# Kernel optimization log

Measured on AMD Instinct MI355X. Metric: run time of the kernel, lower is better.

## Reference

```python
import jax, jax.numpy as jnp
import numpy as np

HEADS = 8
DIM_HEAD = 32


def setup_inputs() -> dict:
    key = jax.random.key(0)
    k1, k2, k3, k4 = jax.random.split(key, 4)
    dim, hidden = 256, HEADS * DIM_HEAD
    x = jax.random.normal(k1, (4, dim, 48, 48), dtype=jnp.float32)
    # 1x1 conv weights stored as [out_ch, in_ch]
    w_qkv = jax.random.normal(k2, (3 * hidden, dim), dtype=jnp.float32) * (dim ** -0.5)
    w_out = jax.random.normal(k3, (dim, hidden), dtype=jnp.float32) * (hidden ** -0.5)
    b_out = jax.random.normal(k4, (dim,), dtype=jnp.float32) * 0.01
    return {"x": x, "w_qkv": w_qkv, "w_out": w_out, "b_out": b_out}


def reference(x, w_qkv, w_out, b_out):
    B, C, H, W = x.shape
    n = H * W
    scale = DIM_HEAD ** -0.5
    # 1x1 conv QKV projection: [B, 3*hidden, H, W] -> [B, 3, heads, dh, n]
    qkv = jnp.einsum('oc,bchw->bohw', w_qkv, x).reshape(B, 3, HEADS, DIM_HEAD, n)
    q, k, v = qkv[:, 0], qkv[:, 1], qkv[:, 2]  # each [B, h, dh, n]
    sim = jnp.einsum('bhdi,bhdj->bhij', q, k) * scale  # [B, h, n, n]
    attn = jax.nn.softmax(sim, axis=-1)
    out = jnp.einsum('bhij,bhdj->bhdi', attn, v)  # [B, h, dh, n] -> channels (h d)
    out = out.reshape(B, HEADS * DIM_HEAD, H, W)
    return jnp.einsum('oc,bchw->bohw', w_out, out) + b_out[None, :, None, None]
```

## Files before the change

### kernel.cpp

```cpp
#include <hip/hip_runtime.h>
#include <hip/hip_bf16.h>

#define NSP 2304
#define NB  4

typedef unsigned short u16;
typedef __attribute__((ext_vector_type(8))) short short8;
typedef __attribute__((ext_vector_type(4))) float f32x4;
typedef __attribute__((ext_vector_type(4))) unsigned short u16x4;

#define K1S 0.25508040852656425f

static __device__ inline u16 f2bf(float f) {
  return __builtin_bit_cast(unsigned short, __float2bfloat16(f));
}
static __device__ inline unsigned cvtpk(float a, float b) {
  unsigned r;
  asm("v_cvt_pk_bf16_f32 %0, %1, %2" : "=v"(r) : "v"(a), "v"(b));
  return r;
}

__global__ __launch_bounds__(256) void convert_w(
    const float* __restrict__ wq, const float* __restrict__ wo,
    u16* __restrict__ dst) {
  int i = (blockIdx.x * 256 + threadIdx.x) * 4;
  float4 v;
  if (i < 196608) v = *(const float4*)(wq + i);
  else            v = *(const float4*)(wo + (i - 196608));
  u16x4 p = {f2bf(v.x), f2bf(v.y), f2bf(v.z), f2bf(v.w)};
  *(u16x4*)(dst + i) = p;
}

__global__ __launch_bounds__(256) void transpose_x(
    const float* __restrict__ x, u16* __restrict__ xT) {
  __shared__ float tile[32][33];
  const int t = threadIdx.x;
  const int n0 = blockIdx.x * 32, c0 = blockIdx.y * 32, b = blockIdx.z;
  const float* xb = x + ((size_t)b * 256 + c0) * NSP + n0;
#pragma unroll
  for (int e = t; e < 1024; e += 256) {
    int cc = e >> 5, nn = e & 31;
    tile[cc][nn] = xb[(size_t)cc * NSP + nn];
  }
  __syncthreads();
  u16* xTb = xT + ((size_t)b * NSP + n0) * 256 + c0;
#pragma unroll
  for (int e = t; e < 1024; e += 256) {
    int nn = e >> 5, cc = e & 31;
    xTb[(size_t)nn * 256 + cc] = f2bf(tile[cc][nn]);
  }
}

template <int EPI>
__global__ __launch_bounds__(256) void gemm_mfma(
    const u16* __restrict__ A, const u16* __restrict__ B,
    u16* __restrict__ qkT, u16* __restrict__ vbuf,
    float* __restrict__ outf, const float* __restrict__ bias, int N) {
  __shared__ u16 As[64][264];
  __shared__ u16 Bs[64][264];
  const int t = threadIdx.x, lane = t & 63, wid = t >> 6;
  const int lo = lane & 15, g = lane >> 4;
  const int wr = wid >> 1, wc = wid & 1;
  const int row0 = blockIdx.y * 64, col0 = blockIdx.x * 64, b = blockIdx.z;

  const int sr = t >> 2, c4 = t & 3;
  const u16* Arow = A + (size_t)(row0 + sr) * 256;
  const u16* Brow = B + ((size_t)b * N + col0 + sr) * 256;
#pragma unroll
  for (int i = 0; i < 8; ++i) {
    int col = (c4 + 4 * i) * 8;
    *(uint4*)&As[sr][col] = *(const uint4*)&Arow[col];
    *(uint4*)&Bs[sr][col] = *(const uint4*)&Brow[col];
  }
  __syncthreads();

  f32x4 acc[2][2];
#pragma unroll
  for (int i = 0; i < 2; ++i)
#pragma unroll
    for (int j = 0; j < 2; ++j) acc[i][j] = (f32x4){0, 0, 0, 0};

  const int ar0 = wr * 32 + lo, br0 = wc * 32 + lo;
#pragma unroll
  for (int kk = 0; kk < 8; ++kk) {
    int kc = kk * 32 + g * 8;
    short8 a0 = *(const short8*)&As[ar0][kc];
    short8 a1 = *(const short8*)&As[ar0 + 16][kc];
    short8 b0 = *(const short8*)&Bs[br0][kc];
    short8 b1 = *(const short8*)&Bs[br0 + 16][kc];
    acc[0][0] = __builtin_amdgcn_mfma_f32_16x16x32_bf16(a0, b0, acc[0][0], 0, 0, 0);
    acc[0][1] = __builtin_amdgcn_mfma_f32_16x16x32_bf16(a0, b1, acc[0][1], 0, 0, 0);
    acc[1][0] = __builtin_amdgcn_mfma_f32_16x16x32_bf16(a1, b0, acc[1][0], 0, 0, 0);
    acc[1][1] = __builtin_amdgcn_mfma_f32_16x16x32_bf16(a1, b1, acc[1][1], 0, 0, 0);
  }

  const float qs = (EPI == 0 && row0 < 256) ? K1S : 1.0f;
#pragma unroll
  for (int m2 = 0; m2 < 2; ++m2)
#pragma unroll
    for (int n2 = 0; n2 < 2; ++n2) {
      int m = row0 + wr * 32 + m2 * 16 + g * 4;
      int n = col0 + wc * 32 + n2 * 16 + lo;
      if constexpr (EPI == 0) {
        if (row0 < 512) {
          u16x4 pk = {f2bf(acc[m2][n2][0] * qs), f2bf(acc[m2][n2][1] * qs),
                      f2bf(acc[m2][n2][2] * qs), f2bf(acc[m2][n2][3] * qs)};
          *(u16x4*)(qkT + ((size_t)b * NSP + n) * 512 + m) = pk;
        } else {
#pragma unroll
          for (int r = 0; r < 4; ++r)
            vbuf[((size_t)b * 256 + (m - 512 + r)) * NSP + n] =
                f2bf(acc[m2][n2][r]);
        }
      } else {
#pragma unroll
        for (int r = 0; r < 4; ++r)
          outf[((size_t)b * 256 + m + r) * NSP + n] =
              acc[m2][n2][r] + bias[m + r];
      }
    }
}

__global__ __launch_bounds__(128, 2) void attn_mfma(
    const u16* __restrict__ qkT, const u16* __restrict__ vbuf,
    u16* __restrict__ attnoT) {
  const int jb = blockIdx.x;
  const int h = jb & 7;
  const int qq = jb >> 3;
  const int it = qq % 24;
  const int b  = qq / 24;
  const int t = threadIdx.x, lane = t & 63, w = t >> 6;
  const int lo = lane & 15, g = lane >> 4;
  const int i0 = it * 96;

  const u16* qkTb = qkT + (size_t)b * NSP * 512;
  const u16* vb   = vbuf + ((size_t)b * 256 + h * 32) * NSP;
  u16* ob = attnoT + ((size_t)b * NSP + i0) * 256 + h * 32;

  __shared__ u16 Kt[2][128][42];
  __shared__ u16 Vs[2][32][138];

  short8 qf[3];
#pragma unroll
  for (int qh = 0; qh < 3; ++qh)
    qf[qh] = *(const short8*)(qkTb +
              (size_t)(i0 + w * 48 + qh * 16 + lo) * 512 + h * 32 + g * 8);

  const int kr = t >> 2, kp = (t & 3) * 8;
  const int vr = t >> 4, vjp = (t & 15) * 8;
  const int pc0 = (vjp & ~31) | (8 * ((vjp >> 2) & 3) + 4 * ((vjp >> 4) & 1));
  const u16* ksrc = qkTb + 256 + h * 32 + kp;
  const u16* vsrc = vb + (size_t)vr * NSP + vjp;

  uint4 kv[4], vv[4];
#pragma unroll
  for (int i = 0; i < 4; ++i) {
    kv[i] = *(const uint4*)(ksrc + (size_t)(kr + 32 * i) * 512);
    vv[i] = *(const uint4*)(vsrc + (size_t)(8 * i) * NSP);
  }
#pragma unroll
  for (int i = 0; i < 4; ++i) {
    *(uint4*)&Kt[0][kr + 32 * i][kp] = kv[i];
    *(uint2*)&Vs[0][vr + 8 * i][pc0]     = make_uint2(vv[i].x, vv[i].y);
    *(uint2*)&Vs[0][vr + 8 * i][pc0 + 8] = make_uint2(vv[i].z, vv[i].w);
  }
  __syncthreads();

  short8 ones;
#pragma unroll
  for (int e = 0; e < 8; ++e) ones[e] = (short)0x3F80;

  f32x4 a0[3], a1[3], al[3];
#pragma unroll
  for (int qh = 0; qh < 3; ++qh) {
    a0[qh] = (f32x4){0, 0, 0, 0};
    a1[qh] = (f32x4){0, 0, 0, 0};
    al[qh] = (f32x4){0, 0, 0, 0};
  }

  for (int s = 0; s < 18; ++s) {
    const int cur = s & 1;
    if (s + 1 < 18) {
      const int j0n = (s + 1) * 128;
#pragma unroll
      for (int i = 0; i < 4; ++i) {
        kv[i] = *(const uint4*)(ksrc + (size_t)(j0n + kr + 32 * i) * 512);
        vv[i] = *(const uint4*)(vsrc + j0n + (size_t)(8 * i) * NSP);
      }
    }

#pragma unroll
    for (int h2 = 0; h2 < 2; ++h2) {
      short8 kf0 = *(const short8*)&Kt[cur][h2 * 64 + lo][g * 8];
      short8 kf1 = *(const short8*)&Kt[cur][h2 * 64 + 16 + lo][g * 8];
      short8 kf2 = *(const short8*)&Kt[cur][h2 * 64 + 32 + lo][g * 8];
      short8 kf3 = *(const short8*)&Kt[cur][h2 * 64 + 48 + lo][g * 8];
      short8 vf00 = *(const short8*)&Vs[cur][lo][h2 * 64 + 8 * g];
      short8 vf01 = *(const short8*)&Vs[cur][lo][h2 * 64 + 32 + 8 * g];
      short8 vf10 = *(const short8*)&Vs[cur][16 + lo][h2 * 64 + 8 * g];
      short8 vf11 = *(const short8*)&Vs[cur][16 + lo][h2 * 64 + 32 + 8 * g];

#pragma unroll
      for (int qh = 0; qh < 3; ++qh) {
        __builtin_amdgcn_s_setprio(1);
        f32x4 sv0 = __builtin_amdgcn_mfma_f32_16x16x32_bf16(kf0, qf[qh], (f32x4){0,0,0,0}, 0, 0, 0);
        f32x4 sv1 = __builtin_amdgcn_mfma_f32_16x16x32_bf16(kf1, qf[qh], (f32x4){0,0,0,0}, 0, 0, 0);
        f32x4 sv2 = __builtin_amdgcn_mfma_f32_16x16x32_bf16(kf2, qf[qh], (f32x4){0,0,0,0}, 0, 0, 0);
        f32x4 sv3 = __builtin_amdgcn_mfma_f32_16x16x32_bf16(kf3, qf[qh], (f32x4){0,0,0,0}, 0, 0, 0);
        __builtin_amdgcn_s_setprio(0);

        f32x4 e0, e1, e2, e3;
#pragma unroll
        for (int r = 0; r < 4; ++r) {
          e0[r] = __builtin_amdgcn_exp2f(sv0[r]);
          e1[r] = __builtin_amdgcn_exp2f(sv1[r]);
          e2[r] = __builtin_amdgcn_exp2f(sv2[r]);
          e3[r] = __builtin_amdgcn_exp2f(sv3[r]);
        }
        uint4 P0 = {cvtpk(e0[0], e0[1]), cvtpk(e0[2], e0[3]),
                    cvtpk(e1[0], e1[1]), cvtpk(e1[2], e1[3])};
        uint4 P1 = {cvtpk(e2[0], e2[1]), cvtpk(e2[2], e2[3]),
                    cvtpk(e3[0], e3[1]), cvtpk(e3[2], e3[3])};
        short8 pf0 = __builtin_bit_cast(short8, P0);
        short8 pf1 = __builtin_bit_cast(short8, P1);

        __builtin_amdgcn_s_setprio(1);
        a0[qh] = __builtin_amdgcn_mfma_f32_16x16x32_bf16(pf0, vf00, a0[qh], 0, 0, 0);
        a1[qh] = __builtin_amdgcn_mfma_f32_16x16x32_bf16(pf0, vf10, a1[qh], 0, 0, 0);
        al[qh] = __builtin_amdgcn_mfma_f32_16x16x32_bf16(pf0, ones, al[qh], 0, 0, 0);
        a0[qh] = __builtin_amdgcn_mfma_f32_16x16x32_bf16(pf1, vf01, a0[qh], 0, 0, 0);
        a1[qh] = __builtin_amdgcn_mfma_f32_16x16x32_bf16(pf1, vf11, a1[qh], 0, 0, 0);
        al[qh] = __builtin_amdgcn_mfma_f32_16x16x32_bf16(pf1, ones, al[qh], 0, 0, 0);
        __builtin_amdgcn_s_setprio(0);
      }
    }

    if (s + 1 < 18) {
#pragma unroll
      for (int i = 0; i < 4; ++i) {
        *(uint4*)&Kt[cur ^ 1][kr + 32 * i][kp] = kv[i];
        *(uint2*)&Vs[cur ^ 1][vr + 8 * i][pc0]     = make_uint2(vv[i].x, vv[i].y);
        *(uint2*)&Vs[cur ^ 1][vr + 8 * i][pc0 + 8] = make_uint2(vv[i].z, vv[i].w);
      }
    }
    __syncthreads();
  }

#pragma unroll
  for (int qh = 0; qh < 3; ++qh)
#pragma unroll
    for (int r = 0; r < 4; ++r) {
      float inv = 1.0f / al[qh][r];
      int row = w * 48 + qh * 16 + g * 4 + r;
      ob[(size_t)row * 256 + lo]      = f2bf(a0[qh][r] * inv);
      ob[(size_t)row * 256 + 16 + lo] = f2bf(a1[qh][r] * inv);
    }
}

extern "C" void kernel_launch(void* const* d_in, const int* in_sizes, int n_in,
                              void* d_out, int out_size, void* d_ws, size_t ws_size,
                              hipStream_t stream) {
  const float* x     = (const float*)d_in[0];
  const float* w_qkv = (const float*)d_in[1];
  const float* w_out = (const float*)d_in[2];
  const float* b_out = (const float*)d_in[3];
  float* out = (float*)d_out;

  u16* wbf    = (u16*)d_ws;
  u16* xT     = wbf + 262144;
  u16* qkT    = xT + (size_t)NB * NSP * 256;
  u16* vbuf   = qkT + (size_t)NB * NSP * 512;
  u16* attnoT = vbuf + (size_t)NB * 256 * NSP;

  dim3 blk(256);
  convert_w<<<256, blk, 0, stream>>>(w_qkv, w_out, wbf);
  transpose_x<<<dim3(NSP / 32, 8, NB), blk, 0, stream>>>(x, xT);
  gemm_mfma<0><<<dim3(NSP / 64, 12, NB), blk, 0, stream>>>(
      wbf, xT, qkT, vbuf, nullptr, nullptr, NSP);
  attn_mfma<<<dim3(768), dim3(128), 0, stream>>>(qkT, vbuf, attnoT);
  gemm_mfma<1><<<dim3(NSP / 64, 4, NB), blk, 0, stream>>>(
      wbf + 196608, attnoT, nullptr, nullptr, out, b_out, NSP);
}
```

Before: 75.62 us.

## Swizzle attention LDS tiles with XOR and drop LDS double buffering

Replaces the padded, double-buffered K and V shared-memory tiles with single unpadded buffers. Bank conflicts are now avoided with an XOR swizzle on row and column, which cuts the shared-memory footprint. Next-tile global loads still go to registers early. Writing them to LDS now needs an extra barrier before the store, so the LDS store no longer overlaps the previous tile's compute without a block-wide sync. This trades lower LDS use and possibly cleaner bank access for an extra __syncthreads per iteration.

```diff
diff --git a/kernel.cpp b/kernel.cpp
--- a/kernel.cpp
+++ b/kernel.cpp
@@ -121,6 +121,9 @@
     }
 }
 
+#define KIDX(r, c) ((((r) * 64) + (c)) ^ (((r) & 7) << 3))
+#define VIDX(r, c) ((((r) * 128) + (c)) ^ (((r) & 7) << 3))
+
 __global__ __launch_bounds__(128, 2) void attn_mfma(
     const u16* __restrict__ qkT, const u16* __restrict__ vbuf,
     u16* __restrict__ attnoT) {
@@ -137,8 +140,8 @@
   const u16* vb   = vbuf + ((size_t)b * 256 + h * 32) * NSP;
   u16* ob = attnoT + ((size_t)b * NSP + i0) * 256 + h * 32;
 
-  __shared__ u16 Kt[2][128][42];
-  __shared__ u16 Vs[2][32][138];
+  __shared__ u16 Kt[128 * 64];
+  __shared__ u16 Vs[32 * 128];
 
   short8 qf[3];
 #pragma unroll
@@ -148,7 +151,7 @@
 
   const int kr = t >> 2, kp = (t & 3) * 8;
   const int vr = t >> 4, vjp = (t & 15) * 8;
-  const int pc0 = (vjp & ~31) | (8 * ((vjp >> 2) & 3) + 4 * ((vjp >> 4) & 1));
+  const int pc0 = (vjp & ~31) | (((vjp >> 2) & 3) << 3) | (((vjp >> 4) & 1) << 2);
   const u16* ksrc = qkTb + 256 + h * 32 + kp;
   const u16* vsrc = vb + (size_t)vr * NSP + vjp;
 
@@ -160,9 +163,9 @@
   }
 #pragma unroll
   for (int i = 0; i < 4; ++i) {
-    *(uint4*)&Kt[0][kr + 32 * i][kp] = kv[i];
-    *(uint2*)&Vs[0][vr + 8 * i][pc0]     = make_uint2(vv[i].x, vv[i].y);
-    *(uint2*)&Vs[0][vr + 8 * i][pc0 + 8] = make_uint2(vv[i].z, vv[i].w);
+    *(uint4*)&Kt[KIDX(kr + 32 * i, kp)] = kv[i];
+    *(uint2*)&Vs[VIDX(vr + 8 * i, pc0)]     = make_uint2(vv[i].x, vv[i].y);
+    *(uint2*)&Vs[VIDX(vr + 8 * i, pc0 + 8)] = make_uint2(vv[i].z, vv[i].w);
   }
   __syncthreads();
 
@@ -179,7 +182,6 @@
   }
 
   for (int s = 0; s < 18; ++s) {
-    const int cur = s & 1;
     if (s + 1 < 18) {
       const int j0n = (s + 1) * 128;
 #pragma unroll
@@ -191,14 +193,14 @@
 
 #pragma unroll
     for (int h2 = 0; h2 < 2; ++h2) {
-      short8 kf0 = *(const short8*)&Kt[cur][h2 * 64 + lo][g * 8];
-      short8 kf1 = *(const short8*)&Kt[cur][h2 * 64 + 16 + lo][g * 8];
-      short8 kf2 = *(const short8*)&Kt[cur][h2 * 64 + 32 + lo][g * 8];
-      short8 kf3 = *(const short8*)&Kt[cur][h2 * 64 + 48 + lo][g * 8];
-      short8 vf00 = *(const short8*)&Vs[cur][lo][h2 * 64 + 8 * g];
-      short8 vf01 = *(const short8*)&Vs[cur][lo][h2 * 64 + 32 + 8 * g];
-      short8 vf10 = *(const short8*)&Vs[cur][16 + lo][h2 * 64 + 8 * g];
-      short8 vf11 = *(const short8*)&Vs[cur][16 + lo][h2 * 64 + 32 + 8 * g];
+      short8 kf0 = *(const short8*)&Kt[KIDX(h2 * 64 + lo, g * 8)];
+      short8 kf1 = *(const short8*)&Kt[KIDX(h2 * 64 + 16 + lo, g * 8)];
+      short8 kf2 = *(const short8*)&Kt[KIDX(h2 * 64 + 32 + lo, g * 8)];
+      short8 kf3 = *(const short8*)&Kt[KIDX(h2 * 64 + 48 + lo, g * 8)];
+      short8 vf00 = *(const short8*)&Vs[VIDX(lo, h2 * 64 + 8 * g)];
+      short8 vf01 = *(const short8*)&Vs[VIDX(lo, h2 * 64 + 32 + 8 * g)];
+      short8 vf10 = *(const short8*)&Vs[VIDX(16 + lo, h2 * 64 + 8 * g)];
+      short8 vf11 = *(const short8*)&Vs[VIDX(16 + lo, h2 * 64 + 32 + 8 * g)];
 
 #pragma unroll
       for (int qh = 0; qh < 3; ++qh) {
@@ -236,14 +238,15 @@
     }
 
     if (s + 1 < 18) {
+      __syncthreads();
 #pragma unroll
       for (int i = 0; i < 4; ++i) {
-        *(uint4*)&Kt[cur ^ 1][kr + 32 * i][kp] = kv[i];
-        *(uint2*)&Vs[cur ^ 1][vr + 8 * i][pc0]     = make_uint2(vv[i].x, vv[i].y);
-        *(uint2*)&Vs[cur ^ 1][vr + 8 * i][pc0 + 8] = make_uint2(vv[i].z, vv[i].w);
-      }
-    }
-    __syncthreads();
+        *(uint4*)&Kt[KIDX(kr + 32 * i, kp)] = kv[i];
+        *(uint2*)&Vs[VIDX(vr + 8 * i, pc0)]     = make_uint2(vv[i].x, vv[i].y);
+        *(uint2*)&Vs[VIDX(vr + 8 * i, pc0 + 8)] = make_uint2(vv[i].z, vv[i].w);
+      }
+      __syncthreads();
+    }
   }
 
 #pragma unroll
```

Result: slower. 87.27 us (+15.4%).

## Fuse weight conversion and x transpose into GEMM tile loads

Applied to the files above, without the earlier changes.

Removes the separate convert_w and transpose_x kernels and has the projection GEMMs read fp32 weights and fp32 x directly, converting to bf16 and transposing while filling shared memory. This drops two launches and the round trip of the bf16 xT buffer through global memory. In exchange, each GEMM block re-converts its weight tile, and the QKV GEMM reloads x once per row-block of output channels (12 times). The transposed shared-memory stores are narrow and may cause bank conflicts.

```diff
diff --git a/kernel.cpp b/kernel.cpp
--- a/kernel.cpp
+++ b/kernel.cpp
@@ -20,40 +20,10 @@
   return r;
 }
 
-__global__ __launch_bounds__(256) void convert_w(
-    const float* __restrict__ wq, const float* __restrict__ wo,
-    u16* __restrict__ dst) {
-  int i = (blockIdx.x * 256 + threadIdx.x) * 4;
-  float4 v;
-  if (i < 196608) v = *(const float4*)(wq + i);
-  else            v = *(const float4*)(wo + (i - 196608));
-  u16x4 p = {f2bf(v.x), f2bf(v.y), f2bf(v.z), f2bf(v.w)};
-  *(u16x4*)(dst + i) = p;
-}
-
-__global__ __launch_bounds__(256) void transpose_x(
-    const float* __restrict__ x, u16* __restrict__ xT) {
-  __shared__ float tile[32][33];
-  const int t = threadIdx.x;
-  const int n0 = blockIdx.x * 32, c0 = blockIdx.y * 32, b = blockIdx.z;
-  const float* xb = x + ((size_t)b * 256 + c0) * NSP + n0;
-#pragma unroll
-  for (int e = t; e < 1024; e += 256) {
-    int cc = e >> 5, nn = e & 31;
-    tile[cc][nn] = xb[(size_t)cc * NSP + nn];
-  }
-  __syncthreads();
-  u16* xTb = xT + ((size_t)b * NSP + n0) * 256 + c0;
-#pragma unroll
-  for (int e = t; e < 1024; e += 256) {
-    int nn = e >> 5, cc = e & 31;
-    xTb[(size_t)nn * 256 + cc] = f2bf(tile[cc][nn]);
-  }
-}
-
 template <int EPI>
 __global__ __launch_bounds__(256) void gemm_mfma(
-    const u16* __restrict__ A, const u16* __restrict__ B,
+    const float* __restrict__ W, const float* __restrict__ x,
+    const u16* __restrict__ Bbf,
     u16* __restrict__ qkT, u16* __restrict__ vbuf,
     float* __restrict__ outf, const float* __restrict__ bias, int N) {
   __shared__ u16 As[64][264];
@@ -63,14 +33,43 @@
   const int wr = wid >> 1, wc = wid & 1;
   const int row0 = blockIdx.y * 64, col0 = blockIdx.x * 64, b = blockIdx.z;
 
-  const int sr = t >> 2, c4 = t & 3;
-  const u16* Arow = A + (size_t)(row0 + sr) * 256;
-  const u16* Brow = B + ((size_t)b * N + col0 + sr) * 256;
-#pragma unroll
-  for (int i = 0; i < 8; ++i) {
-    int col = (c4 + 4 * i) * 8;
-    *(uint4*)&As[sr][col] = *(const uint4*)&Arow[col];
-    *(uint4*)&Bs[sr][col] = *(const uint4*)&Brow[col];
+  {
+    const int sr = t >> 2, c4 = (t & 3) * 64;
+    const float* Arow = W + (size_t)(row0 + sr) * 256 + c4;
+#pragma unroll
+    for (int i = 0; i < 8; ++i) {
+      float4 va = *(const float4*)(Arow + i * 8);
+      float4 vb = *(const float4*)(Arow + i * 8 + 4);
+      uint4 p = {cvtpk(va.x, va.y), cvtpk(va.z, va.w),
+                 cvtpk(vb.x, vb.y), cvtpk(vb.z, vb.w)};
+      *(uint4*)&As[sr][c4 + i * 8] = p;
+    }
+  }
+  if constexpr (EPI == 0) {
+    const float* xb = x + (size_t)b * 256 * NSP + col0;
+    const int n0 = (t & 15) * 4;
+#pragma unroll
+    for (int ci = 0; ci < 4; ++ci) {
+      int c = ci * 64 + (t >> 4) * 4;
+      float4 r0 = *(const float4*)(xb + (size_t)(c + 0) * NSP + n0);
+      float4 r1 = *(const float4*)(xb + (size_t)(c + 1) * NSP + n0);
+      float4 r2 = *(const float4*)(xb + (size_t)(c + 2) * NSP + n0);
+      float4 r3 = *(const float4*)(xb + (size_t)(c + 3) * NSP + n0);
+      *(u16x4*)&Bs[n0 + 0][c] =
+          (u16x4){f2bf(r0.x), f2bf(r1.x), f2bf(r2.x), f2bf(r3.x)};
+      *(u16x4*)&Bs[n0 + 1][c] =
+          (u16x4){f2bf(r0.y), f2bf(r1.y), f2bf(r2.y), f2bf(r3.y)};
+      *(u16x4*)&Bs[n0 + 2][c] =
+          (u16x4){f2bf(r0.z), f2bf(r1.z), f2bf(r2.z), f2bf(r3.z)};
+      *(u16x4*)&Bs[n0 + 3][c] =
+          (u16x4){f2bf(r0.w), f2bf(r1.w), f2bf(r2.w), f2bf(r3.w)};
+    }
+  } else {
+    const int sr = t >> 2, c4 = (t & 3) * 64;
+    const u16* Brow = Bbf + ((size_t)b * N + col0 + sr) * 256 + c4;
+#pragma unroll
+    for (int i = 0; i < 8; ++i)
+      *(uint4*)&Bs[sr][c4 + i * 8] = *(const uint4*)(Brow + i * 8);
   }
   __syncthreads();
 
@@ -266,18 +265,14 @@
   const float* b_out = (const float*)d_in[3];
   float* out = (float*)d_out;
 
-  u16* wbf    = (u16*)d_ws;
-  u16* xT     = wbf + 262144;
-  u16* qkT    = xT + (size_t)NB * NSP * 256;
+  u16* qkT    = (u16*)d_ws;
   u16* vbuf   = qkT + (size_t)NB * NSP * 512;
   u16* attnoT = vbuf + (size_t)NB * 256 * NSP;
 
   dim3 blk(256);
-  convert_w<<<256, blk, 0, stream>>>(w_qkv, w_out, wbf);
-  transpose_x<<<dim3(NSP / 32, 8, NB), blk, 0, stream>>>(x, xT);
   gemm_mfma<0><<<dim3(NSP / 64, 12, NB), blk, 0, stream>>>(
-      wbf, xT, qkT, vbuf, nullptr, nullptr, NSP);
+      w_qkv, x, nullptr, qkT, vbuf, nullptr, nullptr, NSP);
   attn_mfma<<<dim3(768), dim3(128), 0, stream>>>(qkT, vbuf, attnoT);
   gemm_mfma<1><<<dim3(NSP / 64, 4, NB), blk, 0, stream>>>(
-      wbf + 196608, attnoT, nullptr, nullptr, out, b_out, NSP);
-}
+      w_out, nullptr, attnoT, nullptr, nullptr, out, b_out, NSP);
+}
```

New measurement: 83.36 us. +10.2%, slower.

## Split attention over key halves and merge partial results in separate kernel

Applied to the files above, without the earlier changes.

Each attention block now processes half of the key sequence, doubling the grid to improve CU occupancy and reduce the wave-quantization tail. Unnormalized fp32 accumulators and row sums are written to a workspace buffer. A new merge kernel sums the two halves, normalizes, and writes bf16 output. This adds extra global memory traffic and a kernel launch.

```diff
diff --git a/kernel.cpp b/kernel.cpp
--- a/kernel.cpp
+++ b/kernel.cpp
@@ -123,22 +123,25 @@
 
 __global__ __launch_bounds__(128, 2) void attn_mfma(
     const u16* __restrict__ qkT, const u16* __restrict__ vbuf,
-    u16* __restrict__ attnoT) {
+    float* __restrict__ part) {
   const int jb = blockIdx.x;
-  const int h = jb & 7;
-  const int qq = jb >> 3;
-  const int it = qq % 24;
-  const int b  = qq / 24;
+  const int h  = jb & 7;
+  const int q2 = jb >> 3;
+  const int kp = q2 & 1;
+  const int q3 = q2 >> 1;
+  const int it = q3 % 24;
+  const int b  = q3 / 24;
+  const int grp = q3 * 8 + h;
   const int t = threadIdx.x, lane = t & 63, w = t >> 6;
   const int lo = lane & 15, g = lane >> 4;
   const int i0 = it * 96;
+  const int j0base = kp * 1152;
 
   const u16* qkTb = qkT + (size_t)b * NSP * 512;
   const u16* vb   = vbuf + ((size_t)b * 256 + h * 32) * NSP;
-  u16* ob = attnoT + ((size_t)b * NSP + i0) * 256 + h * 32;
-
-  __shared__ u16 Kt[2][128][42];
-  __shared__ u16 Vs[2][32][138];
+
+  __shared__ u16 Kt[2][64][40];
+  __shared__ u16 Vs[2][32][70];
 
   short8 qf[3];
 #pragma unroll
@@ -146,24 +149,23 @@
     qf[qh] = *(const short8*)(qkTb +
               (size_t)(i0 + w * 48 + qh * 16 + lo) * 512 + h * 32 + g * 8);
 
-  const int kr = t >> 2, kp = (t & 3) * 8;
-  const int vr = t >> 4, vjp = (t & 15) * 8;
+  const int kr = t >> 2, kpd = (t & 3) * 8;
+  const int vr = t >> 3, vjp = (t & 7) * 8;
   const int pc0 = (vjp & ~31) | (8 * ((vjp >> 2) & 3) + 4 * ((vjp >> 4) & 1));
-  const u16* ksrc = qkTb + 256 + h * 32 + kp;
+  const u16* ksrc = qkTb + 256 + h * 32 + kpd;
   const u16* vsrc = vb + (size_t)vr * NSP + vjp;
 
-  uint4 kv[4], vv[4];
-#pragma unroll
-  for (int i = 0; i < 4; ++i) {
-    kv[i] = *(const uint4*)(ksrc + (size_t)(kr + 32 * i) * 512);
-    vv[i] = *(const uint4*)(vsrc + (size_t)(8 * i) * NSP);
-  }
-#pragma unroll
-  for (int i = 0; i < 4; ++i) {
-    *(uint4*)&Kt[0][kr + 32 * i][kp] = kv[i];
-    *(uint2*)&Vs[0][vr + 8 * i][pc0]     = make_uint2(vv[i].x, vv[i].y);
-    *(uint2*)&Vs[0][vr + 8 * i][pc0 + 8] = make_uint2(vv[i].z, vv[i].w);
-  }
+  uint4 kv[2], vv[2];
+  kv[0] = *(const uint4*)(ksrc + (size_t)(j0base + kr) * 512);
+  kv[1] = *(const uint4*)(ksrc + (size_t)(j0base + kr + 32) * 512);
+  vv[0] = *(const uint4*)(vsrc + j0base);
+  vv[1] = *(const uint4*)(vsrc + j0base + (size_t)16 * NSP);
+  *(uint4*)&Kt[0][kr][kpd]      = kv[0];
+  *(uint4*)&Kt[0][kr + 32][kpd] = kv[1];
+  *(uint2*)&Vs[0][vr][pc0]           = make_uint2(vv[0].x, vv[0].y);
+  *(uint2*)&Vs[0][vr][pc0 + 8]       = make_uint2(vv[0].z, vv[0].w);
+  *(uint2*)&Vs[0][vr + 16][pc0]      = make_uint2(vv[1].x, vv[1].y);
+  *(uint2*)&Vs[0][vr + 16][pc0 + 8]  = make_uint2(vv[1].z, vv[1].w);
   __syncthreads();
 
   short8 ones;
@@ -181,80 +183,98 @@
   for (int s = 0; s < 18; ++s) {
     const int cur = s & 1;
     if (s + 1 < 18) {
-      const int j0n = (s + 1) * 128;
-#pragma unroll
-      for (int i = 0; i < 4; ++i) {
-        kv[i] = *(const uint4*)(ksrc + (size_t)(j0n + kr + 32 * i) * 512);
-        vv[i] = *(const uint4*)(vsrc + j0n + (size_t)(8 * i) * NSP);
+      const int j0n = j0base + (s + 1) * 64;
+      kv[0] = *(const uint4*)(ksrc + (size_t)(j0n + kr) * 512);
+      kv[1] = *(const uint4*)(ksrc + (size_t)(j0n + kr + 32) * 512);
+      vv[0] = *(const uint4*)(vsrc + j0n);
+      vv[1] = *(const uint4*)(vsrc + j0n + (size_t)16 * NSP);
+    }
+
+    short8 kf0 = *(const short8*)&Kt[cur][lo][g * 8];
+    short8 kf1 = *(const short8*)&Kt[cur][16 + lo][g * 8];
+    short8 kf2 = *(const short8*)&Kt[cur][32 + lo][g * 8];
+    short8 kf3 = *(const short8*)&Kt[cur][48 + lo][g * 8];
+    short8 vf00 = *(const short8*)&Vs[cur][lo][8 * g];
+    short8 vf01 = *(const short8*)&Vs[cur][lo][32 + 8 * g];
+    short8 vf10 = *(const short8*)&Vs[cur][16 + lo][8 * g];
+    short8 vf11 = *(const short8*)&Vs[cur][16 + lo][32 + 8 * g];
+
+#pragma unroll
+    for (int qh = 0; qh < 3; ++qh) {
+      __builtin_amdgcn_s_setprio(1);
+      f32x4 sv0 = __builtin_amdgcn_mfma_f32_16x16x32_bf16(kf0, qf[qh], (f32x4){0,0,0,0}, 0, 0, 0);
+      f32x4 sv1 = __builtin_amdgcn_mfma_f32_16x16x32_bf16(kf1, qf[qh], (f32x4){0,0,0,0}, 0, 0, 0);
+      f32x4 sv2 = __builtin_amdgcn_mfma_f32_16x16x32_bf16(kf2, qf[qh], (f32x4){0,0,0,0}, 0, 0, 0);
+      f32x4 sv3 = __builtin_amdgcn_mfma_f32_16x16x32_bf16(kf3, qf[qh], (f32x4){0,0,0,0}, 0, 0, 0);
+      __builtin_amdgcn_s_setprio(0);
+
+      f32x4 e0, e1, e2, e3;
+#pragma unroll
+      for (int r = 0; r < 4; ++r) {
+        e0[r] = __builtin_amdgcn_exp2f(sv0[r]);
+        e1[r] = __builtin_amdgcn_exp2f(sv1[r]);
+        e2[r] = __builtin_amdgcn_exp2f(sv2[r]);
+        e3[r] = __builtin_amdgcn_exp2f(sv3[r]);
       }
-    }
-
-#pragma unroll
-    for (int h2 = 0; h2 < 2; ++h2) {
-      short8 kf0 = *(const short8*)&Kt[cur][h2 * 64 + lo][g * 8];
-      short8 kf1 = *(const short8*)&Kt[cur][h2 * 64 + 16 + lo][g * 8];
-      short8 kf2 = *(const short8*)&Kt[cur][h2 * 64 + 32 + lo][g * 8];
-      short8 kf3 = *(const short8*)&Kt[cur][h2 * 64 + 48 + lo][g * 8];
-      short8 vf00 = *(const short8*)&Vs[cur][lo][h2 * 64 + 8 * g];
-      short8 vf01 = *(const short8*)&Vs[cur][lo][h2 * 64 + 32 + 8 * g];
-      short8 vf10 = *(const short8*)&Vs[cur][16 + lo][h2 * 64 + 8 * g];
-      short8 vf11 = *(const short8*)&Vs[cur][16 + lo][h2 * 64 + 32 + 8 * g];
-
-#pragma unroll
-      for (int qh = 0; qh < 3; ++qh) {
-        __builtin_amdgcn_s_setprio(1);
-        f32x4 sv0 = __builtin_amdgcn_mfma_f32_16x16x32_bf16(kf0, qf[qh], (f32x4){0,0,0,0}, 0, 0, 0);
-        f32x4 sv1 = __builtin_amdgcn_mfma_f32_16x16x32_bf16(kf1, qf[qh], (f32x4){0,0,0,0}, 0, 0, 0);
-        f32x4 sv2 = __builtin_amdgcn_mfma_f32_16x16x32_bf16(kf2, qf[qh], (f32x4){0,0,0,0}, 0, 0, 0);
-        f32x4 sv3 = __builtin_amdgcn_mfma_f32_16x16x32_bf16(kf3, qf[qh], (f32x4){0,0,0,0}, 0, 0, 0);
-        __builtin_amdgcn_s_setprio(0);
-
-        f32x4 e0, e1, e2, e3;
-#pragma unroll
-        for (int r = 0; r < 4; ++r) {
-          e0[r] = __builtin_amdgcn_exp2f(sv0[r]);
-          e1[r] = __builtin_amdgcn_exp2f(sv1[r]);
-          e2[r] = __builtin_amdgcn_exp2f(sv2[r]);
-          e3[r] = __builtin_amdgcn_exp2f(sv3[r]);
-        }
-        uint4 P0 = {cvtpk(e0[0], e0[1]), cvtpk(e0[2], e0[3]),
-                    cvtpk(e1[0], e1[1]), cvtpk(e1[2], e1[3])};
-        uint4 P1 = {cvtpk(e2[0], e2[1]), cvtpk(e2[2], e2[3]),
-                    cvtpk(e3[0], e3[1]), cvtpk(e3[2], e3[3])};
-        short8 pf0 = __builtin_bit_cast(short8, P0);
-        short8 pf1 = __builtin_bit_cast(short8, P1);
-
-        __builtin_amdgcn_s_setprio(1);
-        a0[qh] = __builtin_amdgcn_mfma_f32_16x16x32_bf16(pf0, vf00, a0[qh], 0, 0, 0);
-        a1[qh] = __builtin_amdgcn_mfma_f32_16x16x32_bf16(pf0, vf10, a1[qh], 0, 0, 0);
-        al[qh] = __builtin_amdgcn_mfma_f32_16x16x32_bf16(pf0, ones, al[qh], 0, 0, 0);
-        a0[qh] = __builtin_amdgcn_mfma_f32_16x16x32_bf16(pf1, vf01, a0[qh], 0, 0, 0);
-        a1[qh] = __builtin_amdgcn_mfma_f32_16x16x32_bf16(pf1, vf11, a1[qh], 0, 0, 0);
-        al[qh] = __builtin_amdgcn_mfma_f32_16x16x32_bf16(pf1, ones, al[qh], 0, 0, 0);
-        __builtin_amdgcn_s_setprio(0);
-      }
+      uint4 P0 = {cvtpk(e0[0], e0[1]), cvtpk(e0[2], e0[3]),
+                  cvtpk(e1[0], e1[1]), cvtpk(e1[2], e1[3])};
+      uint4 P1 = {cvtpk(e2[0], e2[1]), cvtpk(e2[2], e2[3]),
+                  cvtpk(e3[0], e3[1]), cvtpk(e3[2], e3[3])};
+      short8 pf0 = __builtin_bit_cast(short8, P0);
+      short8 pf1 = __builtin_bit_cast(short8, P1);
+
+      __builtin_amdgcn_s_setprio(1);
+      a0[qh] = __builtin_amdgcn_mfma_f32_16x16x32_bf16(pf0, vf00, a0[qh], 0, 0, 0);
+      a1[qh] = __builtin_amdgcn_mfma_f32_16x16x32_bf16(pf0, vf10, a1[qh], 0, 0, 0);
+      al[qh] = __builtin_amdgcn_mfma_f32_16x16x32_bf16(pf0, ones, al[qh], 0, 0, 0);
+      a0[qh] = __builtin_amdgcn_mfma_f32_16x16x32_bf16(pf1, vf01, a0[qh], 0, 0, 0);
+      a1[qh] = __builtin_amdgcn_mfma_f32_16x16x32_bf16(pf1, vf11, a1[qh], 0, 0, 0);
+      al[qh] = __builtin_amdgcn_mfma_f32_16x16x32_bf16(pf1, ones, al[qh], 0, 0, 0);
+      __builtin_amdgcn_s_setprio(0);
     }
 
     if (s + 1 < 18) {
-#pragma unroll
-      for (int i = 0; i < 4; ++i) {
-        *(uint4*)&Kt[cur ^ 1][kr + 32 * i][kp] = kv[i];
-        *(uint2*)&Vs[cur ^ 1][vr + 8 * i][pc0]     = make_uint2(vv[i].x, vv[i].y);
-        *(uint2*)&Vs[cur ^ 1][vr + 8 * i][pc0 + 8] = make_uint2(vv[i].z, vv[i].w);
-      }
+      *(uint4*)&Kt[cur ^ 1][kr][kpd]      = kv[0];
+      *(uint4*)&Kt[cur ^ 1][kr + 32][kpd] = kv[1];
+      *(uint2*)&Vs[cur ^ 1][vr][pc0]          = make_uint2(vv[0].x, vv[0].y);
+      *(uint2*)&Vs[cur ^ 1][vr][pc0 + 8]      = make_uint2(vv[0].z, vv[0].w);
+      *(uint2*)&Vs[cur ^ 1][vr + 16][pc0]     = make_uint2(vv[1].x, vv[1].y);
+      *(uint2*)&Vs[cur ^ 1][vr + 16][pc0 + 8] = make_uint2(vv[1].z, vv[1].w);
     }
     __syncthreads();
   }
 
-#pragma unroll
-  for (int qh = 0; qh < 3; ++qh)
-#pragma unroll
-    for (int r = 0; r < 4; ++r) {
-      float inv = 1.0f / al[qh][r];
-      int row = w * 48 + qh * 16 + g * 4 + r;
-      ob[(size_t)row * 256 + lo]      = f2bf(a0[qh][r] * inv);
-      ob[(size_t)row * 256 + 16 + lo] = f2bf(a1[qh][r] * inv);
-    }
+  float* pg = part + ((size_t)kp * 768 + grp) * (33 * 96);
+#pragma unroll
+  for (int qh = 0; qh < 3; ++qh) {
+    int row = w * 48 + qh * 16 + g * 4;
+    *(f32x4*)&pg[(size_t)lo * 96 + row]        = a0[qh];
+    *(f32x4*)&pg[(size_t)(16 + lo) * 96 + row] = a1[qh];
+    if (lo == 0) *(f32x4*)&pg[(size_t)32 * 96 + row] = al[qh];
+  }
+}
+
+__global__ __launch_bounds__(128) void merge_attn(
+    const float* __restrict__ part, u16* __restrict__ attnoT) {
+  const int grp = blockIdx.x;
+  const int h = grp & 7, q3 = grp >> 3;
+  const int it = q3 % 24, b = q3 / 24;
+  const int t = threadIdx.x;
+  if (t >= 96) return;
+  const float* p0 = part + (size_t)grp * (33 * 96);
+  const float* p1 = part + ((size_t)768 + grp) * (33 * 96);
+  float inv = 1.0f / (p0[32 * 96 + t] + p1[32 * 96 + t]);
+  u16* ob = attnoT + ((size_t)b * NSP + it * 96 + t) * 256 + h * 32;
+#pragma unroll
+  for (int c4 = 0; c4 < 8; ++c4) {
+    u16x4 o;
+#pragma unroll
+    for (int j = 0; j < 4; ++j) {
+      int c = c4 * 4 + j;
+      o[j] = f2bf((p0[c * 96 + t] + p1[c * 96 + t]) * inv);
+    }
+    *(u16x4*)&ob[c4 * 4] = o;
+  }
 }
 
 extern "C" void kernel_launch(void* const* d_in, const int* in_sizes, int n_in,
@@ -271,13 +291,15 @@
   u16* qkT    = xT + (size_t)NB * NSP * 256;
   u16* vbuf   = qkT + (size_t)NB * NSP * 512;
   u16* attnoT = vbuf + (size_t)NB * 256 * NSP;
+  float* part = (float*)(attnoT + (size_t)NB * NSP * 256);
 
   dim3 blk(256);
   convert_w<<<256, blk, 0, stream>>>(w_qkv, w_out, wbf);
   transpose_x<<<dim3(NSP / 32, 8, NB), blk, 0, stream>>>(x, xT);
   gemm_mfma<0><<<dim3(NSP / 64, 12, NB), blk, 0, stream>>>(
       wbf, xT, qkT, vbuf, nullptr, nullptr, NSP);
-  attn_mfma<<<dim3(768), dim3(128), 0, stream>>>(qkT, vbuf, attnoT);
+  attn_mfma<<<dim3(1536), dim3(128), 0, stream>>>(qkT, vbuf, part);
+  merge_attn<<<dim3(768), dim3(128), 0, stream>>>(part, attnoT);
   gemm_mfma<1><<<dim3(NSP / 64, 4, NB), blk, 0, stream>>>(
       wbf + 196608, attnoT, nullptr, nullptr, out, b_out, NSP);
 }
```

After: 75.45 us. About the same (-0.2%).
